# Kernel optimization log

Measured on AMD Instinct MI355X. Metric: run time of the kernel, lower is better.

Reference implementation:

```python
import jax, jax.numpy as jnp
import numpy as np

NEG_SLOPE = 0.01  # nn.LeakyReLU default

def leaky(x):
    return jnp.where(x >= 0, x, NEG_SLOPE * x)

def setup_inputs() -> dict:
    key = jax.random.key(0)
    ks = jax.random.split(key, 10)
    N, E, IN_DIM, OUT_DIM = 100000, 1600000, 128, 128
    indices = jax.random.randint(ks[0], (2, E), 0, N, dtype=jnp.int64 if jax.config.jax_enable_x64 else jnp.int32)
    features = jax.random.normal(ks[1], (N, IN_DIM), dtype=jnp.float32)
    s = 1.0 / np.sqrt(IN_DIM)
    W_att_w = jax.random.uniform(ks[2], (OUT_DIM, IN_DIM), minval=-s, maxval=s)
    W_att_b = jax.random.uniform(ks[3], (OUT_DIM,), minval=-s, maxval=s)
    W1_w = jax.random.uniform(ks[4], (OUT_DIM, IN_DIM), minval=-s, maxval=s)
    W1_b = jax.random.uniform(ks[5], (OUT_DIM,), minval=-s, maxval=s)
    W2_w = jax.random.uniform(ks[6], (OUT_DIM, OUT_DIM), minval=-s, maxval=s)
    W2_b = jax.random.uniform(ks[7], (OUT_DIM,), minval=-s, maxval=s)
    # xavier_uniform for a: gain*sqrt(6/(fan_in+fan_out)), fan_in=2*OUT_DIM, fan_out=1
    lim = float(np.sqrt(6.0 / (2 * OUT_DIM + 1)))
    a = jax.random.uniform(ks[8], (2 * OUT_DIM, 1), minval=-lim, maxval=lim)
    return {"indices": indices, "features": features, "num_nodes": N,
            "W_att_w": W_att_w, "W_att_b": W_att_b, "W1_w": W1_w, "W1_b": W1_b,
            "W2_w": W2_w, "W2_b": W2_b, "a": a}

def reference(indices, features, num_nodes, W_att_w, W_att_b, W1_w, W1_b, W2_w, W2_b, a):
    src, dst = indices[0], indices[1]
    out_dim = W_att_w.shape[0]
    # h_trans = W_att(features)
    h_trans = features @ W_att_w.T + W_att_b  # [N, D]
    # cat([src_h, dst_h]) @ a  ==  src_h @ a[:D] + dst_h @ a[D:]  (avoids materializing cat)
    a_src, a_dst = a[:out_dim], a[out_dim:]
    logits = leaky(h_trans[src] @ a_src + h_trans[dst] @ a_dst)  # [E, 1]
    # edge softmax over incoming edges of each dst (raw exp, as in original)
    exp_l = jnp.exp(logits)
    denom = jax.ops.segment_sum(exp_l, dst, num_segments=num_nodes)  # [N, 1]
    alpha = exp_l / (denom[dst] + 1e-9)  # [E, 1]
    # sparse.mm(adj_att, W1(features)) == segment_sum of alpha * msg[src] over dst
    h_msg = features @ W1_w.T + W1_b  # [N, D]
    h_neigh = jax.ops.segment_sum(alpha * h_msg[src], dst, num_segments=num_nodes)  # [N, D]
    h_self = features  # in_dim == out_dim branch
    term1 = h_self + h_neigh
    term2 = (h_self * h_neigh) @ W2_w.T + W2_b
    return leaky(term1 + term2)
```

## Files before the change

kernel.cpp:

```cpp
#include <hip/hip_runtime.h>

#define D 128
typedef __attribute__((ext_vector_type(8))) short short8;
typedef __attribute__((ext_vector_type(4))) float f32x4;

__device__ __forceinline__ float leaky(float x){ return x >= 0.f ? x : 0.01f*x; }
__device__ __forceinline__ unsigned short f2bf(float x){
    unsigned u = __float_as_uint(x);
    u = (u + 0x7fffu + ((u>>16)&1u)) >> 16;
    return (unsigned short)u;
}

__global__ void k_prep(const float* __restrict__ Ww, const float* __restrict__ Wb,
                       const float* __restrict__ a, float* __restrict__ v,
                       const float* __restrict__ W1, const float* __restrict__ W2,
                       unsigned short* __restrict__ W1b, unsigned short* __restrict__ W2b){
    int b = blockIdx.x;
    if(b < 64){
        int i = b*256 + threadIdx.x;
        W1b[i] = f2bf(W1[i]);
        W2b[i] = f2bf(W2[i]);
        return;
    }
    int i = threadIdx.x; if(i >= 128) return;
    float vs=0.f, vd=0.f;
    for (int o=0;o<D;++o){ float w = Ww[o*D+i]; vs = fmaf(w, a[o], vs); vd = fmaf(w, a[D+o], vd); }
    v[i]=vs; v[D+i]=vd;
    if(i==0){
        float cs=0.f,cd=0.f;
        for(int o=0;o<D;++o){ cs=fmaf(Wb[o],a[o],cs); cd=fmaf(Wb[o],a[D+o],cd); }
        v[256]=cs; v[257]=cd;
    }
}

__global__ __launch_bounds__(256) void k_msgscal(const float* __restrict__ F,
        const unsigned short* __restrict__ W1b, const float* __restrict__ b1,
        const float* __restrict__ v, unsigned short* __restrict__ Hp,
        float* __restrict__ ss, float* __restrict__ sd, int N){
    const int lane = threadIdx.x & 63;
    const int wid  = blockIdx.x*4 + (threadIdx.x>>6);
    const int nw   = gridDim.x*4;
    const int t = lane & 15, g = lane >> 4;
    short8 wf[4][8];
    #pragma unroll
    for(int kk=0;kk<4;++kk)
      #pragma unroll
      for(int j=0;j<8;++j)
        wf[kk][j] = *(const short8*)(W1b + (size_t)(j*16+t)*D + kk*32 + g*8);
    float bb[8];
    #pragma unroll
    for(int j=0;j<8;++j) bb[j] = b1[j*16+t];
    const float c_s = v[256], c_d = v[257];
    const int Mt = (N+15)>>4;
    for(int rt = wid; rt < Mt; rt += nw){
        int row0 = rt*16 + t;
        int row = row0 < N ? row0 : N-1;
        const float* fr = F + (size_t)row*D + g*8;
        f32x4 acc[8];
        #pragma unroll
        for(int j=0;j<8;++j) acc[j] = (f32x4){0.f,0.f,0.f,0.f};
        float ds = 0.f, dd = 0.f;
        #pragma unroll
        for(int kk=0;kk<4;++kk){
            f32x4 lo = *(const f32x4*)(fr + kk*32);
            f32x4 hi = *(const f32x4*)(fr + kk*32 + 4);
            f32x4 vsl = *(const f32x4*)(v + kk*32 + g*8);
            f32x4 vsh = *(const f32x4*)(v + kk*32 + g*8 + 4);
            f32x4 vdl = *(const f32x4*)(v + D + kk*32 + g*8);
            f32x4 vdh = *(const f32x4*)(v + D + kk*32 + g*8 + 4);
            #pragma unroll
            for(int q=0;q<4;++q){
                ds = fmaf(lo[q], vsl[q], ds); ds = fmaf(hi[q], vsh[q], ds);
                dd = fmaf(lo[q], vdl[q], dd); dd = fmaf(hi[q], vdh[q], dd);
            }
            short8 af;
            af[0]=(short)f2bf(lo[0]); af[1]=(short)f2bf(lo[1]);
            af[2]=(short)f2bf(lo[2]); af[3]=(short)f2bf(lo[3]);
            af[4]=(short)f2bf(hi[0]); af[5]=(short)f2bf(hi[1]);
            af[6]=(short)f2bf(hi[2]); af[7]=(short)f2bf(hi[3]);
            #pragma unroll
            for(int j=0;j<8;++j)
                acc[j] = __builtin_amdgcn_mfma_f32_16x16x32_bf16(af, wf[kk][j], acc[j], 0,0,0);
        }
        ds += __shfl_xor(ds,16); ds += __shfl_xor(ds,32);
        dd += __shfl_xor(dd,16); dd += __shfl_xor(dd,32);
        if(g==0 && row0 < N){ ss[row0] = ds + c_s; sd[row0] = dd + c_d; }
        #pragma unroll
        for(int r=0;r<4;++r){
            int rr = rt*16 + g*4 + r;
            if(rr < N){
                short8 h;
                #pragma unroll
                for(int j=0;j<8;++j) h[j] = (short)f2bf(acc[j][r] + bb[j]);
                *(short8*)(Hp + (size_t)rr*D + t*8) = h;
            }
        }
    }
}

__global__ __launch_bounds__(256) void k_bcount(const int* __restrict__ dst,
        unsigned* __restrict__ M, int E, int NB, int CHUNK){
    __shared__ unsigned h[1600];
    for(int i=threadIdx.x;i<NB;i+=256) h[i]=0u;
    __syncthreads();
    int s = blockIdx.x*CHUNK;
    int e = s+CHUNK < E ? s+CHUNK : E;
    for(int i=s+(int)threadIdx.x;i<e;i+=256) atomicAdd(&h[((unsigned)dst[i])>>6],1u);
    __syncthreads();
    for(int i=threadIdx.x;i<NB;i+=256) M[(size_t)i*gridDim.x + blockIdx.x] = h[i];
}

__global__ __launch_bounds__(256) void k_scanA(const unsigned* __restrict__ M,
        unsigned* __restrict__ bsum, int n){
    __shared__ unsigned lds[4];
    int base = blockIdx.x*4096 + threadIdx.x*16;
    unsigned s=0;
    #pragma unroll
    for(int k=0;k<16;++k){ int i=base+k; if(i<n) s+=M[i]; }
    #pragma unroll
    for(int o=1;o<64;o<<=1) s += __shfl_xor(s,o);
    if((threadIdx.x&63)==0) lds[threadIdx.x>>6]=s;
    __syncthreads();
    if(threadIdx.x==0) bsum[blockIdx.x] = lds[0]+lds[1]+lds[2]+lds[3];
}

__global__ __launch_bounds__(256) void k_scanB(unsigned* __restrict__ bsum, int nb){
    __shared__ unsigned lds[4];
    int t = threadIdx.x;
    int chunk = (nb+255)/256;
    int s0 = t*chunk, s1 = s0+chunk < nb ? s0+chunk : nb;
    unsigned tsum=0;
    for(int i=s0;i<s1;++i) tsum += bsum[i];
    unsigned x=tsum;
    #pragma unroll
    for(int o=1;o<64;o<<=1){ unsigned y=__shfl_up(x,(unsigned)o); if((t&63)>=o) x+=y; }
    if((t&63)==63) lds[t>>6]=x;
    __syncthreads();
    unsigned woff=0;
    for(int w=0;w<(t>>6);++w) woff+=lds[w];
    unsigned run = woff + (x - tsum);
    for(int i=s0;i<s1;++i){ unsigned vv=bsum[i]; bsum[i]=run; run+=vv; }
}

__global__ __launch_bounds__(256) void k_scanC(const unsigned* __restrict__ M,
        const unsigned* __restrict__ bsum, unsigned* __restrict__ Msc, int n){
    __shared__ unsigned lds[4];
    int t = threadIdx.x;
    int base = blockIdx.x*4096 + t*16;
    unsigned v[16]; unsigned tsum=0;
    #pragma unroll
    for(int k=0;k<16;++k){ int i=base+k; v[k]=(i<n)?M[i]:0u; tsum+=v[k]; }
    unsigned x=tsum;
    #pragma unroll
    for(int o=1;o<64;o<<=1){ unsigned y=__shfl_up(x,(unsigned)o); if((t&63)>=o) x+=y; }
    if((t&63)==63) lds[t>>6]=x;
    __syncthreads();
    unsigned woff = bsum[blockIdx.x];
    for(int w=0;w<(t>>6);++w) woff+=lds[w];
    unsigned run = woff + (x - tsum);
    #pragma unroll
    for(int k=0;k<16;++k){ int i=base+k; if(i<n) Msc[i]=run; run+=v[k]; }
}

__global__ __launch_bounds__(256) void k_bscatter(const int* __restrict__ src,
        const int* __restrict__ dst, const unsigned* __restrict__ Msc,
        uint2* __restrict__ ew, int E, int NB, int CHUNK){
    __shared__ unsigned hoff[1600];
    int blk = blockIdx.x, NBLKg = gridDim.x;
    for(int i=threadIdx.x;i<NB;i+=256) hoff[i] = Msc[(size_t)i*NBLKg + blk];
    __syncthreads();
    int s = blk*CHUNK;
    int e = s+CHUNK < E ? s+CHUNK : E;
    for(int i=s+(int)threadIdx.x;i<e;i+=256){
        int d = dst[i];
        unsigned p = atomicAdd(&hoff[((unsigned)d)>>6], 1u);
        ew[p] = make_uint2((unsigned)src[i], (unsigned)d);
    }
}

__global__ __launch_bounds__(256) void k_fine(const uint2* __restrict__ ew,
        const unsigned* __restrict__ Msc, unsigned* __restrict__ esrc,
        unsigned* __restrict__ offs, int N, int NB, int NBLKg, int E){
    __shared__ unsigned cA[64], cB[64], loff[64];
    __shared__ unsigned begS, endS;
    int b = blockIdx.x;
    int dbase = b<<6;
    if(threadIdx.x==0){
        begS = Msc[(size_t)b*NBLKg];
        endS = (b+1 < NB) ? Msc[(size_t)(b+1)*NBLKg] : (unsigned)E;
    }
    if(threadIdx.x<64){ cA[threadIdx.x]=0u; cB[threadIdx.x]=0u; }
    __syncthreads();
    const unsigned beg = begS, end = endS;
    for(unsigned i=beg+threadIdx.x; i<end; i+=256)
        atomicAdd(&cA[ew[i].y & 63], 1u);
    __syncthreads();
    if(threadIdx.x<64){
        unsigned c = cA[threadIdx.x];
        unsigned x = c;
        #pragma unroll
        for(int o=1;o<64;o<<=1){ unsigned y = __shfl_up(x,(unsigned)o); if((int)threadIdx.x>=o) x += y; }
        loff[threadIdx.x] = x - c;
        int dd = dbase + (int)threadIdx.x;
        if(dd < N) offs[dd] = beg + x - c;
    }
    if(b==0 && threadIdx.x==64) offs[N] = (unsigned)E;
    __syncthreads();
    for(unsigned i=beg+threadIdx.x; i<end; i+=256){
        uint2 p = ew[i];
        unsigned dl = p.y & 63;
        unsigned r = atomicAdd(&cB[dl], 1u);
        esrc[beg + loff[dl] + r] = p.x;
    }
}

__global__ __launch_bounds__(256) void k_gather(const unsigned* __restrict__ off,
        const unsigned* __restrict__ esrc, const float* __restrict__ ss,
        const float* __restrict__ sdv, const unsigned short* __restrict__ Hp,
        float* __restrict__ out, int N){
    const int wv = threadIdx.x>>6, l = threadIdx.x&63;
    const int d = blockIdx.x*4 + wv;
    if(d>=N) return;
    const int g = l>>4, t = l&15;
    const unsigned kb = off[d], ke = off[d+1];
    const float sdd = sdv[d];
    float acc[8];
    #pragma unroll
    for(int j=0;j<8;++j) acc[j]=0.f;
    float den = 0.f;

    unsigned eA = kb + g;
    unsigned eB = eA + 4;
    bool vA = eA < ke, vB = eB < ke;
    float ssA=0.f, ssB=0.f;
    uint4 uA = make_uint4(0u,0u,0u,0u), uB = make_uint4(0u,0u,0u,0u);
    if(vA){ unsigned s=esrc[eA]; ssA=ss[s]; uA=*(const uint4*)(Hp+(size_t)s*D+t*8); }
    if(vB){ unsigned s=esrc[eB]; ssB=ss[s]; uB=*(const uint4*)(Hp+(size_t)s*D+t*8); }
    while(vA){
        unsigned eC = eB + 4;
        bool vC = eC < ke;
        float ssC = 0.f; uint4 uC = make_uint4(0u,0u,0u,0u);
        if(vC){ unsigned s=esrc[eC]; ssC=ss[s]; uC=*(const uint4*)(Hp+(size_t)s*D+t*8); }
        float w = __expf(leaky(ssA + sdd));
        acc[0] = fmaf(w, __uint_as_float(uA.x<<16),        acc[0]);
        acc[1] = fmaf(w, __uint_as_float(uA.x&0xffff0000u),acc[1]);
        acc[2] = fmaf(w, __uint_as_float(uA.y<<16),        acc[2]);
        acc[3] = fmaf(w, __uint_as_float(uA.y&0xffff0000u),acc[3]);
        acc[4] = fmaf(w, __uint_as_float(uA.z<<16),        acc[4]);
        acc[5] = fmaf(w, __uint_as_float(uA.z&0xffff0000u),acc[5]);
        acc[6] = fmaf(w, __uint_as_float(uA.w<<16),        acc[6]);
        acc[7] = fmaf(w, __uint_as_float(uA.w&0xffff0000u),acc[7]);
        den += w;
        vA = vB; ssA = ssB; uA = uB;
        vB = vC; ssB = ssC; uB = uC;
        eB = eC;
    }
    #pragma unroll
    for(int j=0;j<8;++j){
        acc[j] += __shfl_xor(acc[j],16);
        acc[j] += __shfl_xor(acc[j],32);
    }
    den += __shfl_xor(den,16);
    den += __shfl_xor(den,32);
    float inv = 1.f/(den + 1e-9f);
    int c = g*32 + t;
    out[(size_t)d*D + c]      = acc[g*2]  * inv;
    out[(size_t)d*D + c + 16] = acc[g*2+1]* inv;
}

__global__ __launch_bounds__(256) void k_final(const float* __restrict__ F,
        const unsigned short* __restrict__ W2b, const float* __restrict__ b2,
        float* __restrict__ out, int N){
    const int lane = threadIdx.x & 63;
    const int wid  = blockIdx.x*4 + (threadIdx.x>>6);
    const int nw   = gridDim.x*4;
    const int t = lane & 15, g = lane >> 4;
    short8 wf[4][8];
    #pragma unroll
    for(int kk=0;kk<4;++kk)
      #pragma unroll
      for(int j=0;j<8;++j)
        wf[kk][j] = *(const short8*)(W2b + (size_t)(j*16+t)*D + kk*32 + g*8);
    float bb[8];
    #pragma unroll
    for(int j=0;j<8;++j) bb[j] = b2[j*16+t];
    const int Mt = (N+15)>>4;
    for(int rt = wid; rt < Mt; rt += nw){
        int row = rt*16 + t; if(row>=N) row = N-1;
        const float* fr = F   + (size_t)row*D + g*8;
        const float* hr = out + (size_t)row*D + g*8;
        f32x4 acc[8];
        #pragma unroll
        for(int j=0;j<8;++j) acc[j] = (f32x4){0.f,0.f,0.f,0.f};
        #pragma unroll
        for(int kk=0;kk<4;++kk){
            f32x4 flo = *(const f32x4*)(fr + kk*32);
            f32x4 fhi = *(const f32x4*)(fr + kk*32 + 4);
            f32x4 hlo = *(const f32x4*)(hr + kk*32);
            f32x4 hhi = *(const f32x4*)(hr + kk*32 + 4);
            short8 af;
            af[0]=(short)f2bf(flo[0]*hlo[0]); af[1]=(short)f2bf(flo[1]*hlo[1]);
            af[2]=(short)f2bf(flo[2]*hlo[2]); af[3]=(short)f2bf(flo[3]*hlo[3]);
            af[4]=(short)f2bf(fhi[0]*hhi[0]); af[5]=(short)f2bf(fhi[1]*hhi[1]);
            af[6]=(short)f2bf(fhi[2]*hhi[2]); af[7]=(short)f2bf(fhi[3]*hhi[3]);
            #pragma unroll
            for(int j=0;j<8;++j)
                acc[j] = __builtin_amdgcn_mfma_f32_16x16x32_bf16(af, wf[kk][j], acc[j], 0,0,0);
        }
        #pragma unroll
        for(int r=0;r<4;++r){
            int rr = rt*16 + g*4 + r;
            if(rr < N){
                #pragma unroll
                for(int j=0;j<8;++j){
                    int c = j*16 + t;
                    float f = F[(size_t)rr*D + c];
                    float h = out[(size_t)rr*D + c];
                    float val = f + h + acc[j][r] + bb[j];
                    out[(size_t)rr*D + c] = leaky(val);
                }
            }
        }
    }
}

extern "C" void kernel_launch(void* const* d_in, const int* in_sizes, int n_in,
                              void* d_out, int out_size, void* d_ws, size_t ws_size,
                              hipStream_t stream) {
    const int*   idx  = (const int*)  d_in[0];
    const float* F    = (const float*)d_in[1];
    const float* Waw  = (const float*)d_in[3];
    const float* Wab  = (const float*)d_in[4];
    const float* W1w  = (const float*)d_in[5];
    const float* W1b  = (const float*)d_in[6];
    const float* W2w  = (const float*)d_in[7];
    const float* W2b  = (const float*)d_in[8];
    const float* a    = (const float*)d_in[9];
    float* out = (float*)d_out;

    const int E = in_sizes[0]/2;
    const int N = in_sizes[1]/D;
    const int* srcp = idx;
    const int* dstp = idx + E;

    const int NBLK = 256;
    const int CHUNK = (E + NBLK - 1)/NBLK;
    const int NB = (N + 63)/64;
    const int NT = NB*NBLK;
    const int NSB = (NT + 4095)/4096;

    unsigned short* Hp  = (unsigned short*)d_ws;
    unsigned short* W1c = Hp + (size_t)N*D;
    unsigned short* W2c = W1c + 16384;
    float*    ss   = (float*)(W2c + 16384);
    float*    sd   = ss + N;
    float*    v    = sd + N;
    unsigned* M    = (unsigned*)(v + 320);
    unsigned* Msc  = M + NT;
    unsigned* bsum = Msc + NT + 2;
    unsigned* offs = bsum + NSB + 2;
    unsigned* esrc = offs + (N+2);
    uint2*    ew   = (uint2*)(esrc + E + 2);

    k_prep    <<<65, 256, 0, stream>>>(Waw, Wab, a, v, W1w, W2w, W1c, W2c);
    k_msgscal <<<512, 256, 0, stream>>>(F, W1c, W1b, v, Hp, ss, sd, N);
    k_bcount  <<<NBLK, 256, 0, stream>>>(dstp, M, E, NB, CHUNK);
    k_scanA   <<<NSB, 256, 0, stream>>>(M, bsum, NT);
    k_scanB   <<<1, 256, 0, stream>>>(bsum, NSB);
    k_scanC   <<<NSB, 256, 0, stream>>>(M, bsum, Msc, NT);
    k_bscatter<<<NBLK, 256, 0, stream>>>(srcp, dstp, Msc, ew, E, NB, CHUNK);
    k_fine    <<<NB, 256, 0, stream>>>(ew, Msc, esrc, offs, N, NB, NBLK, E);
    k_gather  <<<(N+3)/4, 256, 0, stream>>>(offs, esrc, ss, sd, Hp, out, N);
    k_final   <<<512, 256, 0, stream>>>(F, W2c, W2b, out, N);
}
```

Measured before the change: 202.8 us.

## Precompute edge weights in CSR build and simplify gather loop

Edge attention weights exp(leaky(ss[src]+sd[dst])) are now computed once in k_fine and stored alongside the source index as a packed (src, weight) pair. The gather kernel no longer does a dependent ss[src] load or an exp per edge. Its loop is restructured to handle two edges per iteration with unconditional prefetching, relying on zero padding written past E. The workspace layout is reordered, and the msgscal and final kernels get a grid sized to the node count instead of a fixed 512 blocks. The cost is wider 8-byte CSR entries and extra work in k_fine.

```diff
diff --git a/kernel.cpp b/kernel.cpp
--- a/kernel.cpp
+++ b/kernel.cpp
@@ -179,9 +179,11 @@
 }
 
 __global__ __launch_bounds__(256) void k_fine(const uint2* __restrict__ ew,
-        const unsigned* __restrict__ Msc, unsigned* __restrict__ esrc,
+        const unsigned* __restrict__ Msc, const float* __restrict__ ss,
+        const float* __restrict__ sdv, uint2* __restrict__ ewp,
         unsigned* __restrict__ offs, int N, int NB, int NBLKg, int E){
     __shared__ unsigned cA[64], cB[64], loff[64];
+    __shared__ float sdl[64];
     __shared__ unsigned begS, endS;
     int b = blockIdx.x;
     int dbase = b<<6;
@@ -189,7 +191,11 @@
         begS = Msc[(size_t)b*NBLKg];
         endS = (b+1 < NB) ? Msc[(size_t)(b+1)*NBLKg] : (unsigned)E;
     }
-    if(threadIdx.x<64){ cA[threadIdx.x]=0u; cB[threadIdx.x]=0u; }
+    if(threadIdx.x<64){
+        cA[threadIdx.x]=0u; cB[threadIdx.x]=0u;
+        int dd = dbase + (int)threadIdx.x;
+        sdl[threadIdx.x] = (dd<N) ? sdv[dd] : 0.f;
+    }
     __syncthreads();
     const unsigned beg = begS, end = endS;
     for(unsigned i=beg+threadIdx.x; i<end; i+=256)
@@ -205,55 +211,59 @@
         if(dd < N) offs[dd] = beg + x - c;
     }
     if(b==0 && threadIdx.x==64) offs[N] = (unsigned)E;
+    if(b==0 && threadIdx.x>=80 && threadIdx.x<96)
+        ewp[E + (threadIdx.x-80)] = make_uint2(0u, 0u);
     __syncthreads();
     for(unsigned i=beg+threadIdx.x; i<end; i+=256){
         uint2 p = ew[i];
         unsigned dl = p.y & 63;
+        float w = __expf(leaky(ss[p.x] + sdl[dl]));
         unsigned r = atomicAdd(&cB[dl], 1u);
-        esrc[beg + loff[dl] + r] = p.x;
-    }
+        ewp[beg + loff[dl] + r] = make_uint2(p.x, __float_as_uint(w));
+    }
+}
+
+__device__ __forceinline__ void fma8(float* acc, uint4 u, float w){
+    acc[0]=fmaf(w,__uint_as_float(u.x<<16),acc[0]);
+    acc[1]=fmaf(w,__uint_as_float(u.x&0xffff0000u),acc[1]);
+    acc[2]=fmaf(w,__uint_as_float(u.y<<16),acc[2]);
+    acc[3]=fmaf(w,__uint_as_float(u.y&0xffff0000u),acc[3]);
+    acc[4]=fmaf(w,__uint_as_float(u.z<<16),acc[4]);
+    acc[5]=fmaf(w,__uint_as_float(u.z&0xffff0000u),acc[5]);
+    acc[6]=fmaf(w,__uint_as_float(u.w<<16),acc[6]);
+    acc[7]=fmaf(w,__uint_as_float(u.w&0xffff0000u),acc[7]);
 }
 
 __global__ __launch_bounds__(256) void k_gather(const unsigned* __restrict__ off,
-        const unsigned* __restrict__ esrc, const float* __restrict__ ss,
-        const float* __restrict__ sdv, const unsigned short* __restrict__ Hp,
+        const uint2* __restrict__ ewp, const unsigned short* __restrict__ Hp,
         float* __restrict__ out, int N){
     const int wv = threadIdx.x>>6, l = threadIdx.x&63;
     const int d = blockIdx.x*4 + wv;
     if(d>=N) return;
     const int g = l>>4, t = l&15;
     const unsigned kb = off[d], ke = off[d+1];
-    const float sdd = sdv[d];
+    const unsigned toff = (unsigned)t*16u;
     float acc[8];
     #pragma unroll
     for(int j=0;j<8;++j) acc[j]=0.f;
     float den = 0.f;
 
-    unsigned eA = kb + g;
-    unsigned eB = eA + 4;
-    bool vA = eA < ke, vB = eB < ke;
-    float ssA=0.f, ssB=0.f;
-    uint4 uA = make_uint4(0u,0u,0u,0u), uB = make_uint4(0u,0u,0u,0u);
-    if(vA){ unsigned s=esrc[eA]; ssA=ss[s]; uA=*(const uint4*)(Hp+(size_t)s*D+t*8); }
-    if(vB){ unsigned s=esrc[eB]; ssB=ss[s]; uB=*(const uint4*)(Hp+(size_t)s*D+t*8); }
-    while(vA){
-        unsigned eC = eB + 4;
-        bool vC = eC < ke;
-        float ssC = 0.f; uint4 uC = make_uint4(0u,0u,0u,0u);
-        if(vC){ unsigned s=esrc[eC]; ssC=ss[s]; uC=*(const uint4*)(Hp+(size_t)s*D+t*8); }
-        float w = __expf(leaky(ssA + sdd));
-        acc[0] = fmaf(w, __uint_as_float(uA.x<<16),        acc[0]);
-        acc[1] = fmaf(w, __uint_as_float(uA.x&0xffff0000u),acc[1]);
-        acc[2] = fmaf(w, __uint_as_float(uA.y<<16),        acc[2]);
-        acc[3] = fmaf(w, __uint_as_float(uA.y&0xffff0000u),acc[3]);
-        acc[4] = fmaf(w, __uint_as_float(uA.z<<16),        acc[4]);
-        acc[5] = fmaf(w, __uint_as_float(uA.z&0xffff0000u),acc[5]);
-        acc[6] = fmaf(w, __uint_as_float(uA.w<<16),        acc[6]);
-        acc[7] = fmaf(w, __uint_as_float(uA.w&0xffff0000u),acc[7]);
-        den += w;
-        vA = vB; ssA = ssB; uA = uB;
-        vB = vC; ssB = ssC; uB = uC;
-        eB = eC;
+    unsigned e = kb + g;
+    uint2 p0 = ewp[e];
+    uint4 u0 = *(const uint4*)((const char*)Hp + ((p0.x<<8) + toff));
+    uint2 p1 = ewp[e+4];
+    uint4 u1 = *(const uint4*)((const char*)Hp + ((p1.x<<8) + toff));
+    while(e < ke){
+        float w0 = __uint_as_float(p0.y);
+        fma8(acc, u0, w0);
+        p0 = ewp[e+8];
+        u0 = *(const uint4*)((const char*)Hp + ((p0.x<<8) + toff));
+        float w1 = (e+4 < ke) ? __uint_as_float(p1.y) : 0.f;
+        fma8(acc, u1, w1);
+        p1 = ewp[e+12];
+        u1 = *(const uint4*)((const char*)Hp + ((p1.x<<8) + toff));
+        den += w0 + w1;
+        e += 8;
     }
     #pragma unroll
     for(int j=0;j<8;++j){
@@ -349,7 +359,9 @@
     const int NT = NB*NBLK;
     const int NSB = (NT + 4095)/4096;
 
-    unsigned short* Hp  = (unsigned short*)d_ws;
+    uint2*    ew   = (uint2*)d_ws;
+    uint2*    ewp  = ew + E;
+    unsigned short* Hp  = (unsigned short*)(ewp + E + 16);
     unsigned short* W1c = Hp + (size_t)N*D;
     unsigned short* W2c = W1c + 16384;
     float*    ss   = (float*)(W2c + 16384);
@@ -359,17 +371,18 @@
     unsigned* Msc  = M + NT;
     unsigned* bsum = Msc + NT + 2;
     unsigned* offs = bsum + NSB + 2;
-    unsigned* esrc = offs + (N+2);
-    uint2*    ew   = (uint2*)(esrc + E + 2);
+
+    const int Mt = (N+15)/16;
+    const int GG = (Mt+7)/8;
 
     k_prep    <<<65, 256, 0, stream>>>(Waw, Wab, a, v, W1w, W2w, W1c, W2c);
-    k_msgscal <<<512, 256, 0, stream>>>(F, W1c, W1b, v, Hp, ss, sd, N);
+    k_msgscal <<<GG, 256, 0, stream>>>(F, W1c, W1b, v, Hp, ss, sd, N);
     k_bcount  <<<NBLK, 256, 0, stream>>>(dstp, M, E, NB, CHUNK);
     k_scanA   <<<NSB, 256, 0, stream>>>(M, bsum, NT);
     k_scanB   <<<1, 256, 0, stream>>>(bsum, NSB);
     k_scanC   <<<NSB, 256, 0, stream>>>(M, bsum, Msc, NT);
     k_bscatter<<<NBLK, 256, 0, stream>>>(srcp, dstp, Msc, ew, E, NB, CHUNK);
-    k_fine    <<<NB, 256, 0, stream>>>(ew, Msc, esrc, offs, N, NB, NBLK, E);
-    k_gather  <<<(N+3)/4, 256, 0, stream>>>(offs, esrc, ss, sd, Hp, out, N);
-    k_final   <<<512, 256, 0, stream>>>(F, W2c, W2b, out, N);
-}
+    k_fine    <<<NB, 256, 0, stream>>>(ew, Msc, ss, sd, ewp, offs, N, NB, NBLK, E);
+    k_gather  <<<(N+3)/4, 256, 0, stream>>>(offs, ewp, Hp, out, N);
+    k_final   <<<GG, 256, 0, stream>>>(F, W2c, W2b, out, N);
+}
```

Measured after the change: 220.8 us. 1.09x slower.
